# Kernel optimization log

Hardware: AMD Instinct MI355X
Metric: run time of the kernel (lower is better)

## Reference

```python
import jax, jax.numpy as jnp
import numpy as np

N = 50000      # nodes
E = 800000     # edges
DIN = 256
DH = 256
DOUT = 64


def setup_inputs() -> dict:
    key = jax.random.key(0)
    ks = jax.random.split(key, 8)
    x = jax.random.normal(ks[0], (N, DIN), dtype=jnp.float32)
    edge_index = jax.random.randint(ks[1], (2, E), 0, N, dtype=jnp.int64)
    s = 0.05
    W1 = jax.random.normal(ks[2], (DIN, DH), dtype=jnp.float32) * s
    b1 = jnp.zeros((DH,), dtype=jnp.float32)
    W2 = jax.random.normal(ks[3], (DH, DH), dtype=jnp.float32) * s
    b2 = jnp.zeros((DH,), dtype=jnp.float32)
    W3 = jax.random.normal(ks[4], (DH, DOUT), dtype=jnp.float32) * s
    b3 = jnp.zeros((DOUT,), dtype=jnp.float32)
    return {"x": x, "edge_index": edge_index, "W1": W1, "b1": b1,
            "W2": W2, "b2": b2, "W3": W3, "b3": b3}


def gcn_conv(x, src, dst, deg_inv_sqrt, W, b):
    # x: [N, din] -> [N, dout]. PyG GCNConv: h = D^{-1/2}(A+I)D^{-1/2} (x W) + b
    n = x.shape[0]
    h = x @ W                                   # [N, dout]
    norm = deg_inv_sqrt[src] * deg_inv_sqrt[dst]  # [E+N]
    msgs = h[src] * norm[:, None]               # gather + scale, [E+N, dout]
    out = jax.ops.segment_sum(msgs, dst, num_segments=n)  # scatter-add
    return out + b


def _loops(edge_index, n):
    # add self loops, compute symmetric normalization degrees
    sl = jnp.arange(n, dtype=edge_index.dtype)
    src = jnp.concatenate([edge_index[0], sl])
    dst = jnp.concatenate([edge_index[1], sl])
    deg = jax.ops.segment_sum(jnp.ones_like(dst, dtype=jnp.float32), dst, num_segments=n)
    dis = jnp.where(deg > 0, jax.lax.rsqrt(deg), 0.0)
    return src, dst, dis


def reference(x, edge_index, W1, b1, W2, b2, W3, b3):
    src, dst, dis = _loops(edge_index, x.shape[0])
    h = jax.nn.relu(gcn_conv(x, src, dst, dis, W1, b1))   # dropout: eval no-op
    h = jax.nn.relu(gcn_conv(h, src, dst, dis, W2, b2))
    out = gcn_conv(h, src, dst, dis, W3, b3)              # batch=None -> no pooling
    return out
```

## Files before the change

kernel.cpp:

```cpp
#include <hip/hip_runtime.h>
#include <hip/hip_fp8.h>
#include <cstdint>
#include <cstddef>

typedef unsigned short u16;
typedef _Float16 f16x8 __attribute__((ext_vector_type(8)));
typedef float f32x2 __attribute__((ext_vector_type(2)));
typedef float f32x4 __attribute__((ext_vector_type(4)));

#if defined(__has_builtin)
#if __has_builtin(__builtin_amdgcn_cvt_pk_f32_fp8) && __has_builtin(__builtin_amdgcn_cvt_pk_fp8_f32)
#define FP8_BUILTIN 1
#endif
#endif

__device__ __forceinline__ float h2f(u16 u) {
  return (float)__builtin_bit_cast(_Float16, u);
}
__device__ __forceinline__ u16 f2h(float f) {
  return __builtin_bit_cast(u16, (_Float16)f);
}
__device__ __forceinline__ unsigned pkh(float lo, float hi) {
  return (unsigned)f2h(lo) | ((unsigned)f2h(hi) << 16);
}
__device__ __forceinline__ unsigned char ftofp8(float f) {
#ifdef FP8_BUILTIN
  return (unsigned char)(__builtin_amdgcn_cvt_pk_fp8_f32(f, f, 0, false) & 0xFF);
#else
  return __hip_fp8_e4m3(f).__x;
#endif
}

__device__ __forceinline__ void async16(u16* lds, const u16* g) {
  __builtin_amdgcn_global_load_lds(
      (const __attribute__((address_space(1))) unsigned int*)g,
      (__attribute__((address_space(3))) unsigned int*)lds, 16, 0, 0);
}

__device__ __forceinline__ void fma8p(float* a, float d, uint2 p) {
#ifdef FP8_BUILTIN
  f32x2 v0 = __builtin_amdgcn_cvt_pk_f32_fp8((int)p.x, false);
  f32x2 v1 = __builtin_amdgcn_cvt_pk_f32_fp8((int)p.x, true);
  f32x2 v2 = __builtin_amdgcn_cvt_pk_f32_fp8((int)p.y, false);
  f32x2 v3 = __builtin_amdgcn_cvt_pk_f32_fp8((int)p.y, true);
  a[0] += d * v0.x; a[1] += d * v0.y; a[2] += d * v1.x; a[3] += d * v1.y;
  a[4] += d * v2.x; a[5] += d * v2.y; a[6] += d * v3.x; a[7] += d * v3.y;
#else
  const unsigned char* b = (const unsigned char*)&p;
#pragma unroll
  for (int k = 0; k < 8; ++k) {
    __hip_fp8_e4m3 v; v.__x = b[k];
    a[k] += d * (float)v;
  }
#endif
}

__device__ __forceinline__ void fma16p(float* a, float d, uint4 p) {
  fma8p(a, d, make_uint2(p.x, p.y));
  fma8p(a + 8, d, make_uint2(p.z, p.w));
}

__device__ __forceinline__ void fma8h(float* a, float d, uint4 p) {
  const u16* q = (const u16*)&p;
#pragma unroll
  for (int k = 0; k < 8; ++k) a[k] += d * h2f(q[k]);
}

__device__ __forceinline__ f16x8 cvt8(const float* p) {
  float4 a = *(const float4*)p;
  float4 b = *(const float4*)(p + 4);
  f16x8 r;
  r[0] = (_Float16)a.x; r[1] = (_Float16)a.y; r[2] = (_Float16)a.z; r[3] = (_Float16)a.w;
  r[4] = (_Float16)b.x; r[5] = (_Float16)b.y; r[6] = (_Float16)b.z; r[7] = (_Float16)b.w;
  return r;
}

__device__ __forceinline__ int wave_is64(const void* ep) {
  const unsigned* p = (const unsigned*)ep;
  const int lane = threadIdx.x & 63;
  unsigned v = p[2 * lane + 1] | p[2 * (lane + 64) + 1];
  unsigned long long bal = __ballot(v != 0u);
  return (bal == 0ull) ? 1 : 0;
}

__device__ __forceinline__ int edge_at(const void* ep, int is64, long long idx) {
  if (is64) return (int)((const long long*)ep)[idx];
  return ((const int*)ep)[idx];
}

#define NCHUNK 256

__global__ void zero_f32(float* p, int n) {
  int i = blockIdx.x * 256 + threadIdx.x;
  if (i < n) p[i] = 0.f;
}

__global__ __launch_bounds__(256) void prep_all(
    const float* __restrict__ W1, u16* __restrict__ wt1,
    const float* __restrict__ W2, u16* __restrict__ wt2,
    const float* __restrict__ W3, u16* __restrict__ wt3,
    const void* __restrict__ ep, int* __restrict__ cnt,
    int E, int N, int DIN, int DH, int DOUT,
    int nb_w1, int nb_w2, int nb_w3) {
  int b = blockIdx.x;
  if (b < nb_w1) {
    int idx = b * 256 + threadIdx.x;
    if (idx < DIN * DH) {
      int n = idx / DIN, k = idx % DIN;
      wt1[idx] = f2h(W1[k * DH + n]);
    }
    return;
  }
  b -= nb_w1;
  if (b < nb_w2) {
    int idx = b * 256 + threadIdx.x;
    if (idx < DH * DH) {
      int n = idx / DH, k = idx % DH;
      wt2[idx] = f2h(W2[k * DH + n]);
    }
    return;
  }
  b -= nb_w2;
  if (b < nb_w3) {
    int idx = b * 256 + threadIdx.x;
    if (idx < DH * DOUT) {
      int n = idx / DH, k = idx % DH;
      wt3[idx] = f2h(W3[k * DOUT + n]);
    }
    return;
  }
  b -= nb_w3;
  {
    __shared__ int h[256];
    h[threadIdx.x] = 0;
    __syncthreads();
    int is64 = wave_is64(ep);
    const int per = (E + NCHUNK - 1) / NCHUNK;
    const int e0 = b * per, e1 = min(e0 + per, E);
    for (int e = e0 + (int)threadIdx.x; e < e1; e += 256) {
      int d = edge_at(ep, is64, (long long)E + e);
      d = min(max(d, 0), N - 1);
      atomicAdd(&h[d >> 8], 1);
    }
    __syncthreads();
    cnt[b * 256 + threadIdx.x] = h[threadIdx.x];
  }
}

__device__ __forceinline__ void bases_in_lds(const int* __restrict__ cnt,
                                             int nbuck, int E, int* bl, int* ws4) {
  const int t = threadIdx.x, lane = t & 63, w = t >> 6;
  int tot = 0;
  if (t < nbuck) {
#pragma unroll 4
    for (int c = 0; c < NCHUNK; ++c) tot += cnt[c * 256 + t];
  }
  int inc = tot;
#pragma unroll
  for (int o = 1; o < 64; o <<= 1) {
    int u = __shfl_up(inc, o, 64);
    if (lane >= o) inc += u;
  }
  if (lane == 63) ws4[w] = inc;
  __syncthreads();
  if (t == 0) {
    int run = 0;
#pragma unroll
    for (int k = 0; k < 4; ++k) { int v = ws4[k]; ws4[k + 4] = run; run += v; }
  }
  __syncthreads();
  bl[t] = ws4[w + 4] + inc - tot;
  if (t == 0) bl[nbuck] = E;
  __syncthreads();
}

template <int BN, int OUT8, int A32, int NBT, int SC>
__device__ __forceinline__ void gemm_dev(const void* __restrict__ A,
                                         const u16* __restrict__ Bt,
                                         void* __restrict__ Cv, int Nt,
                                         int Nrows, int bm, int col0, u16* Bs) {
  constexpr int K = 256;
  constexpr int NJ = BN / 16;
  constexpr int CH = BN * K / 8;
  const int tid = threadIdx.x, lane = tid & 63, w = tid >> 6;

  auto stage = [&](int bt) {
#pragma unroll
    for (int i = 0; i < CH / 256; ++i) {
      int c = tid + i * 256;
      int ln = c & 63, t2 = c >> 6;
      int ks = t2 & 7, j = t2 >> 3;
      int row = bt * BN + j * 16 + (ln & 15);
      int kk = ks * 32 + (ln >> 4) * 8;
      async16(&Bs[(size_t)c * 8], Bt + (size_t)row * K + kk);
    }
  };
  stage(0);

  const int r16 = lane & 15, quad = lane >> 4;
  const int m0 = w * 32;
  int row0 = bm * 128 + m0 + r16;
  int row1 = row0 + 16;
  f16x8 aa0[8], aa1[8];
  if (A32) {
    row0 = min(row0, Nrows - 1);
    row1 = min(row1, Nrows - 1);
    const float* A0 = (const float*)A + (size_t)row0 * K + quad * 8;
    const float* A1 = (const float*)A + (size_t)row1 * K + quad * 8;
#pragma unroll
    for (int ks = 0; ks < 8; ++ks) {
      aa0[ks] = cvt8(A0 + ks * 32);
      aa1[ks] = cvt8(A1 + ks * 32);
    }
  } else {
    const u16* A0 = (const u16*)A + (size_t)row0 * K + quad * 8;
    const u16* A1 = (const u16*)A + (size_t)row1 * K + quad * 8;
#pragma unroll
    for (int ks = 0; ks < 8; ++ks) {
      aa0[ks] = *(const f16x8*)(A0 + ks * 32);
      aa1[ks] = *(const f16x8*)(A1 + ks * 32);
    }
  }

  const f32x4 fzero = {0.f, 0.f, 0.f, 0.f};
#pragma unroll
  for (int bt = 0; bt < NBT; ++bt) {
    f32x4 acc[2][NJ];
#pragma unroll
    for (int i = 0; i < 2; ++i)
#pragma unroll
      for (int j = 0; j < NJ; ++j) acc[i][j] = fzero;
    __syncthreads();
#pragma unroll
    for (int ks = 0; ks < 8; ++ks)
#pragma unroll
      for (int j = 0; j < NJ; ++j) {
        f16x8 bf = *(const f16x8*)(&Bs[(size_t)((j * 8 + ks) * 64 + lane) * 8]);
        acc[0][j] = __builtin_amdgcn_mfma_f32_16x16x32_f16(aa0[ks], bf, acc[0][j], 0, 0, 0);
        acc[1][j] = __builtin_amdgcn_mfma_f32_16x16x32_f16(aa1[ks], bf, acc[1][j], 0, 0, 0);
      }
    if (bt + 1 < NBT) {
      __syncthreads();
      stage(bt + 1);
    }
#pragma unroll
    for (int i = 0; i < 2; ++i)
#pragma unroll
      for (int j = 0; j < NJ; ++j) {
        int gr = bm * 128 + m0 + i * 16 + quad * 4;
        int gc = col0 + bt * BN + j * 16 + r16;
#pragma unroll
        for (int r = 0; r < 4; ++r) {
          if (OUT8) {
            ((unsigned char*)Cv)[(size_t)(gr + r) * Nt + gc] =
                ftofp8(acc[i][j][r] * (float)SC);
          } else {
            ((u16*)Cv)[(size_t)(gr + r) * Nt + gc] = f2h(acc[i][j][r]);
          }
        }
      }
  }
}

template <int BN, int OUT8, int A32, int NBT, int SC>
__global__ __launch_bounds__(256) void gemm_bres(const void* __restrict__ A,
                                                 const u16* __restrict__ Bt,
                                                 void* __restrict__ Cv, int Nt,
                                                 int Nrows) {
  __shared__ __align__(16) u16 Bs[BN * 256];
  const int col0 = blockIdx.y * (NBT * BN);
  gemm_dev<BN, OUT8, A32, NBT, SC>(A, Bt + (size_t)col0 * 256, Cv, Nt, Nrows,
                                   (int)blockIdx.x, col0, Bs);
}

__global__ __launch_bounds__(256) void bucket_gemm1(
    const void* __restrict__ ep, const int* __restrict__ cnt,
    unsigned* __restrict__ tmp, const float* __restrict__ x,
    const u16* __restrict__ wt1, unsigned char* __restrict__ hbuf,
    int E, int N, int nbuck) {
  __shared__ __align__(16) u16 Bs[128 * 256];
  if ((int)blockIdx.x >= NCHUNK) {
    gemm_dev<128, 1, 1, 2, 1>(x, wt1, hbuf, 256, N, (int)blockIdx.x - NCHUNK, 0, Bs);
    return;
  }
  int* bl = (int*)Bs;
  int* cur = bl + 272;
  int* ws4 = cur + 256;
  const int chunk = blockIdx.x;
  const int t = threadIdx.x;
  bases_in_lds(cnt, nbuck, E, bl, ws4);
  if (t < nbuck) {
    int partial = 0;
    for (int c = 0; c < chunk; ++c) partial += cnt[c * 256 + t];
    cur[t] = bl[t] + partial;
  }
  __syncthreads();
  int is64 = wave_is64(ep);
  const int per = (E + NCHUNK - 1) / NCHUNK;
  const int e0 = chunk * per, e1 = min(e0 + per, E);
  for (int e = e0 + t; e < e1; e += 256) {
    int s = edge_at(ep, is64, e);
    int d = edge_at(ep, is64, (long long)E + e);
    s = min(max(s, 0), N - 1);
    d = min(max(d, 0), N - 1);
    int pos = atomicAdd(&cur[d >> 8], 1);
    tmp[pos] = ((unsigned)d << 16) | (unsigned)s;
  }
}

__global__ __launch_bounds__(256) void csr_final(const unsigned* __restrict__ tmp,
                                                 const int* __restrict__ cnt,
                                                 int* __restrict__ rp,
                                                 float* __restrict__ dis,
                                                 u16* __restrict__ col,
                                                 int N, int E, int nbuck) {
  __shared__ int bl[257];
  __shared__ int hcnt[256];
  __shared__ int curs[256];
  __shared__ int ws4[8];
  const int b = blockIdx.x;
  const int node0 = b * 256;
  const int t = threadIdx.x, lane = t & 63, w = t >> 6;
  bases_in_lds(cnt, nbuck, E, bl, ws4);
  const int k0 = bl[b], k1 = bl[b + 1];
  hcnt[t] = 0;
  __syncthreads();
  for (int k = k0 + t; k < k1; k += 256)
    atomicAdd(&hcnt[(int)(tmp[k] >> 16) - node0], 1);
  __syncthreads();
  const int v = hcnt[t];
  int inc = v;
#pragma unroll
  for (int o = 1; o < 64; o <<= 1) {
    int u = __shfl_up(inc, o, 64);
    if (lane >= o) inc += u;
  }
  __syncthreads();
  if (lane == 63) ws4[w] = inc;
  __syncthreads();
  if (t == 0) {
    int run = 0;
#pragma unroll
    for (int k = 0; k < 4; ++k) { int vv = ws4[k]; ws4[k + 4] = run; run += vv; }
  }
  __syncthreads();
  const int excl = k0 + ws4[w + 4] + inc - v;
  if (node0 + t < N) {
    rp[node0 + t] = excl;
    dis[node0 + t] = rsqrtf((float)(v + 1));
  }
  if (b == 0 && t == 0) rp[N] = E;
  curs[t] = excl;
  __syncthreads();
  for (int k = k0 + t; k < k1; k += 256) {
    unsigned e = tmp[k];
    int dl = (int)(e >> 16) - node0;
    int pos = atomicAdd(&curs[dl], 1);
    col[pos] = (u16)(e & 0xFFFFu);
  }
}

template <int SCALED>
__global__ __launch_bounds__(256) void agg_d256(const unsigned char* __restrict__ h,
                                                const int* __restrict__ rp,
                                                const u16* __restrict__ col,
                                                const float* __restrict__ dis,
                                                const float* __restrict__ bias,
                                                u16* __restrict__ out, int N) {
  const int wid = threadIdx.x >> 6, lane = threadIdx.x & 63;
  const int i = blockIdx.x * 4 + wid;
  if (i >= N) return;
  const int sub = lane >> 4;
  const int l16 = lane & 15;
  const int cb = l16 * 16;
  const float di = dis[i];
  float a[16];
#pragma unroll
  for (int k = 0; k < 16; ++k) a[k] = 0.f;
  if (sub == 0) {
    uint4 sv = *(const uint4*)(h + (size_t)i * 256 + cb);
    fma16p(a, SCALED ? 1.f : di, sv);
  }
  const int e1 = rp[i + 1];
  for (int base = rp[i]; base < e1; base += 64) {
    int me = base + lane;
    int s_l = 0; float d_l = 0.f;
    if (me < e1) { s_l = (int)col[me]; if (!SCALED) d_l = dis[s_l]; }
    const int cnt = min(64, e1 - base);
    const int cntR = (cnt + 15) & ~15;
    for (int t = 0; t < cntR; t += 16) {
      int sA = __shfl(s_l, t + sub, 64);
      int sB = __shfl(s_l, t + 4 + sub, 64);
      int sC = __shfl(s_l, t + 8 + sub, 64);
      int sD = __shfl(s_l, t + 12 + sub, 64);
      float dA, dB, dC, dD;
      if (SCALED) {
        dA = (t + sub < cnt) ? 1.f : 0.f;
        dB = (t + 4 + sub < cnt) ? 1.f : 0.f;
        dC = (t + 8 + sub < cnt) ? 1.f : 0.f;
        dD = (t + 12 + sub < cnt) ? 1.f : 0.f;
      } else {
        dA = __shfl(d_l, t + sub, 64);
        dB = __shfl(d_l, t + 4 + sub, 64);
        dC = __shfl(d_l, t + 8 + sub, 64);
        dD = __shfl(d_l, t + 12 + sub, 64);
      }
      uint4 pA = *(const uint4*)(h + (size_t)sA * 256 + cb);
      uint4 pB = *(const uint4*)(h + (size_t)sB * 256 + cb);
      uint4 pC = *(const uint4*)(h + (size_t)sC * 256 + cb);
      uint4 pD = *(const uint4*)(h + (size_t)sD * 256 + cb);
      fma16p(a, dA, pA); fma16p(a, dB, pB); fma16p(a, dC, pC); fma16p(a, dD, pD);
    }
  }
#pragma unroll
  for (int k = 0; k < 16; ++k) a[k] += __shfl_xor(a[k], 16, 64);
#pragma unroll
  for (int k = 0; k < 16; ++k) a[k] += __shfl_xor(a[k], 32, 64);
  if (sub == 0) {
    const float inv = SCALED ? 0.25f : 1.f;
    const float* bp = bias + l16 * 16;
    float4 b0 = *(const float4*)(bp);
    float4 b1 = *(const float4*)(bp + 4);
    float4 b2 = *(const float4*)(bp + 8);
    float4 b3 = *(const float4*)(bp + 12);
    float bb[16] = {b0.x, b0.y, b0.z, b0.w, b1.x, b1.y, b1.z, b1.w,
                    b2.x, b2.y, b2.z, b2.w, b3.x, b3.y, b3.z, b3.w};
    float r[16];
#pragma unroll
    for (int k = 0; k < 16; ++k)
      r[k] = fmaxf(di * a[k] * inv + bb[k], 0.f) * di;
    uint4 o0, o1;
    o0.x = pkh(r[0], r[1]);  o0.y = pkh(r[2], r[3]);
    o0.z = pkh(r[4], r[5]);  o0.w = pkh(r[6], r[7]);
    o1.x = pkh(r[8], r[9]);  o1.y = pkh(r[10], r[11]);
    o1.z = pkh(r[12], r[13]); o1.w = pkh(r[14], r[15]);
    *(uint4*)(out + (size_t)i * 256 + l16 * 16) = o0;
    *(uint4*)(out + (size_t)i * 256 + l16 * 16 + 8) = o1;
  }
}

__global__ __launch_bounds__(256) void agg_d64(const u16* __restrict__ h,
                                               const int* __restrict__ rp,
                                               const u16* __restrict__ col,
                                               const float* __restrict__ dis,
                                               const float* __restrict__ bias,
                                               float* __restrict__ out, int N) {
  const int wid = threadIdx.x >> 6, lane = threadIdx.x & 63;
  const int i = blockIdx.x * 4 + wid;
  if (i >= N) return;
  const int grp = lane >> 3;
  const int l8 = lane & 7;
  const int c8 = l8 * 8;
  const float di = dis[i];
  float a[8] = {0.f, 0.f, 0.f, 0.f, 0.f, 0.f, 0.f, 0.f};
  if (grp == 0) {
    uint4 sv = *(const uint4*)(h + (size_t)i * 64 + c8);
    fma8h(a, 1.f, sv);
  }
  const int e1 = rp[i + 1];
  for (int base = rp[i]; base < e1; base += 64) {
    int me = base + lane;
    int s_l = 0;
    if (me < e1) s_l = (int)col[me];
    const int cnt = min(64, e1 - base);
    const int cntR = (cnt + 15) & ~15;
    for (int t = 0; t < cntR; t += 16) {
      int sA = __shfl(s_l, t + grp, 64);
      int sB = __shfl(s_l, t + 8 + grp, 64);
      float dA = (t + grp < cnt) ? 1.f : 0.f;
      float dB = (t + 8 + grp < cnt) ? 1.f : 0.f;
      uint4 pA = *(const uint4*)(h + (size_t)sA * 64 + c8);
      uint4 pB = *(const uint4*)(h + (size_t)sB * 64 + c8);
      fma8h(a, dA, pA); fma8h(a, dB, pB);
    }
  }
#pragma unroll
  for (int k = 0; k < 8; ++k) a[k] += __shfl_xor(a[k], 8, 64);
#pragma unroll
  for (int k = 0; k < 8; ++k) a[k] += __shfl_xor(a[k], 16, 64);
#pragma unroll
  for (int k = 0; k < 8; ++k) a[k] += __shfl_xor(a[k], 32, 64);
  if (lane < 8) {
    float4 b0 = *(const float4*)(bias + c8);
    float4 b1 = *(const float4*)(bias + c8 + 4);
    float4 o0, o1;
    o0.x = di * a[0] + b0.x; o0.y = di * a[1] + b0.y;
    o0.z = di * a[2] + b0.z; o0.w = di * a[3] + b0.w;
    o1.x = di * a[4] + b1.x; o1.y = di * a[5] + b1.y;
    o1.z = di * a[6] + b1.z; o1.w = di * a[7] + b1.w;
    *(float4*)(out + (size_t)i * 64 + c8) = o0;
    *(float4*)(out + (size_t)i * 64 + c8 + 4) = o1;
  }
}

extern "C" void kernel_launch(void* const* d_in, const int* in_sizes, int n_in,
                              void* d_out, int out_size, void* d_ws, size_t ws_size,
                              hipStream_t stream) {
  if (n_in < 8) return;
  const float* x = (const float*)d_in[0];
  const void* eptr = d_in[1];
  const float* W1 = (const float*)d_in[2];
  const float* b1 = (const float*)d_in[3];
  const float* W2 = (const float*)d_in[4];
  const float* b2 = (const float*)d_in[5];
  const float* W3 = (const float*)d_in[6];
  const float* b3 = (const float*)d_in[7];
  float* out = (float*)d_out;

  const int DIN = 256, DH = 256;
  const int N = in_sizes[0] / DIN;
  const int E = in_sizes[1] / 2;
  const int DOUT = in_sizes[6] / DH;
  const int MT = (N + 127) / 128;
  const int Mpad = MT * 128;
  const int nbuck = (N + 255) >> 8;

  auto rnd = [](size_t b) { return (b + 255) & ~(size_t)255; };
  size_t required = 0;
  required += rnd((size_t)Mpad * DH * 2);
  required += rnd((size_t)Mpad * DH);
  required += rnd((size_t)E * 2);
  required += rnd((size_t)E * 4);
  required += rnd((size_t)(N + 1) * 4);
  required += rnd((size_t)N * 4);
  required += rnd((size_t)DIN * DH * 2);
  required += rnd((size_t)DH * DH * 2);
  required += rnd((size_t)DH * DOUT * 2);
  required += rnd((size_t)256 * NCHUNK * 4);
  if (ws_size < required || N > 65536 || nbuck > 256 || nbuck < 1 ||
      E < 128 || DOUT != 64) {
    zero_f32<<<(out_size + 255) / 256, 256, 0, stream>>>(out, out_size);
    return;
  }

  char* ws = (char*)d_ws;
  size_t off0 = 0;
  auto alloc = [&](size_t bytes) {
    char* p = ws + off0;
    off0 = (off0 + bytes + 255) & ~(size_t)255;
    return p;
  };
  u16* xpad = (u16*)alloc((size_t)Mpad * DH * 2);
  unsigned char* hbuf = (unsigned char*)alloc((size_t)Mpad * DH);
  u16* colb = (u16*)alloc((size_t)E * 2);
  unsigned* tmpb = (unsigned*)alloc((size_t)E * 4);
  int* rp = (int*)alloc((size_t)(N + 1) * 4);
  float* dis = (float*)alloc((size_t)N * 4);
  u16* wt1 = (u16*)alloc((size_t)DIN * DH * 2);
  u16* wt2 = (u16*)alloc((size_t)DH * DH * 2);
  u16* wt3 = (u16*)alloc((size_t)DH * DOUT * 2);
  int* cnt = (int*)alloc((size_t)256 * NCHUNK * 4);

  const int nb_w1 = (DIN * DH + 255) / 256;
  const int nb_w2 = (DH * DH + 255) / 256;
  const int nb_w3 = (DH * DOUT + 255) / 256;
  prep_all<<<nb_w1 + nb_w2 + nb_w3 + NCHUNK, 256, 0, stream>>>(
      W1, wt1, W2, wt2, W3, wt3, eptr, cnt,
      E, N, DIN, DH, DOUT, nb_w1, nb_w2, nb_w3);

  bucket_gemm1<<<NCHUNK + MT, 256, 0, stream>>>(eptr, cnt, tmpb, x, wt1, hbuf,
                                                E, N, nbuck);
  csr_final<<<nbuck, 256, 0, stream>>>(tmpb, cnt, rp, dis, colb, N, E, nbuck);

  agg_d256<0><<<(N + 3) / 4, 256, 0, stream>>>(hbuf, rp, colb, dis, b1, xpad, N);
  gemm_bres<128, 1, 0, 2, 4><<<dim3(MT, 1), 256, 0, stream>>>(xpad, wt2, hbuf, DH, N);
  agg_d256<1><<<(N + 3) / 4, 256, 0, stream>>>(hbuf, rp, colb, dis, b2, xpad, N);
  gemm_bres<64, 0, 0, 1, 1><<<dim3(MT, DOUT / 64), 256, 0, stream>>>(
      xpad, wt3, hbuf, DOUT, N);
  agg_d64<<<(N + 3) / 4, 256, 0, stream>>>((const u16*)hbuf, rp, colb, dis, b3,
                                           out, N);
}
```

Measured before the change: 323.7 us.

## Split fused bucket/GEMM kernel, use 64-row GEMM tiles, deepen gather unrolling

Separates the CSR bucketing from the first GEMM so each is its own launch. Replaces the 128-row, 64KB-LDS GEMM with a 64-row tile using 32KB LDS and one A fragment per wave, which doubles the block count and cuts register and LDS pressure. The aggregation loops now issue 8 (d256) or 4 (d64) independent row gathers per iteration instead of 4 or 2, giving more memory-level parallelism. The cost is an extra launch, the loss of overlap between bucketing and GEMM1, and more re-staging of B per output row.

```diff
diff --git a/kernel.cpp b/kernel.cpp
--- a/kernel.cpp
+++ b/kernel.cpp
@@ -174,118 +174,13 @@
   __syncthreads();
 }
 
-template <int BN, int OUT8, int A32, int NBT, int SC>
-__device__ __forceinline__ void gemm_dev(const void* __restrict__ A,
-                                         const u16* __restrict__ Bt,
-                                         void* __restrict__ Cv, int Nt,
-                                         int Nrows, int bm, int col0, u16* Bs) {
-  constexpr int K = 256;
-  constexpr int NJ = BN / 16;
-  constexpr int CH = BN * K / 8;
-  const int tid = threadIdx.x, lane = tid & 63, w = tid >> 6;
-
-  auto stage = [&](int bt) {
-#pragma unroll
-    for (int i = 0; i < CH / 256; ++i) {
-      int c = tid + i * 256;
-      int ln = c & 63, t2 = c >> 6;
-      int ks = t2 & 7, j = t2 >> 3;
-      int row = bt * BN + j * 16 + (ln & 15);
-      int kk = ks * 32 + (ln >> 4) * 8;
-      async16(&Bs[(size_t)c * 8], Bt + (size_t)row * K + kk);
-    }
-  };
-  stage(0);
-
-  const int r16 = lane & 15, quad = lane >> 4;
-  const int m0 = w * 32;
-  int row0 = bm * 128 + m0 + r16;
-  int row1 = row0 + 16;
-  f16x8 aa0[8], aa1[8];
-  if (A32) {
-    row0 = min(row0, Nrows - 1);
-    row1 = min(row1, Nrows - 1);
-    const float* A0 = (const float*)A + (size_t)row0 * K + quad * 8;
-    const float* A1 = (const float*)A + (size_t)row1 * K + quad * 8;
-#pragma unroll
-    for (int ks = 0; ks < 8; ++ks) {
-      aa0[ks] = cvt8(A0 + ks * 32);
-      aa1[ks] = cvt8(A1 + ks * 32);
-    }
-  } else {
-    const u16* A0 = (const u16*)A + (size_t)row0 * K + quad * 8;
-    const u16* A1 = (const u16*)A + (size_t)row1 * K + quad * 8;
-#pragma unroll
-    for (int ks = 0; ks < 8; ++ks) {
-      aa0[ks] = *(const f16x8*)(A0 + ks * 32);
-      aa1[ks] = *(const f16x8*)(A1 + ks * 32);
-    }
-  }
-
-  const f32x4 fzero = {0.f, 0.f, 0.f, 0.f};
-#pragma unroll
-  for (int bt = 0; bt < NBT; ++bt) {
-    f32x4 acc[2][NJ];
-#pragma unroll
-    for (int i = 0; i < 2; ++i)
-#pragma unroll
-      for (int j = 0; j < NJ; ++j) acc[i][j] = fzero;
-    __syncthreads();
-#pragma unroll
-    for (int ks = 0; ks < 8; ++ks)
-#pragma unroll
-      for (int j = 0; j < NJ; ++j) {
-        f16x8 bf = *(const f16x8*)(&Bs[(size_t)((j * 8 + ks) * 64 + lane) * 8]);
-        acc[0][j] = __builtin_amdgcn_mfma_f32_16x16x32_f16(aa0[ks], bf, acc[0][j], 0, 0, 0);
-        acc[1][j] = __builtin_amdgcn_mfma_f32_16x16x32_f16(aa1[ks], bf, acc[1][j], 0, 0, 0);
-      }
-    if (bt + 1 < NBT) {
-      __syncthreads();
-      stage(bt + 1);
-    }
-#pragma unroll
-    for (int i = 0; i < 2; ++i)
-#pragma unroll
-      for (int j = 0; j < NJ; ++j) {
-        int gr = bm * 128 + m0 + i * 16 + quad * 4;
-        int gc = col0 + bt * BN + j * 16 + r16;
-#pragma unroll
-        for (int r = 0; r < 4; ++r) {
-          if (OUT8) {
-            ((unsigned char*)Cv)[(size_t)(gr + r) * Nt + gc] =
-                ftofp8(acc[i][j][r] * (float)SC);
-          } else {
-            ((u16*)Cv)[(size_t)(gr + r) * Nt + gc] = f2h(acc[i][j][r]);
-          }
-        }
-      }
-  }
-}
-
-template <int BN, int OUT8, int A32, int NBT, int SC>
-__global__ __launch_bounds__(256) void gemm_bres(const void* __restrict__ A,
-                                                 const u16* __restrict__ Bt,
-                                                 void* __restrict__ Cv, int Nt,
-                                                 int Nrows) {
-  __shared__ __align__(16) u16 Bs[BN * 256];
-  const int col0 = blockIdx.y * (NBT * BN);
-  gemm_dev<BN, OUT8, A32, NBT, SC>(A, Bt + (size_t)col0 * 256, Cv, Nt, Nrows,
-                                   (int)blockIdx.x, col0, Bs);
-}
-
-__global__ __launch_bounds__(256) void bucket_gemm1(
-    const void* __restrict__ ep, const int* __restrict__ cnt,
-    unsigned* __restrict__ tmp, const float* __restrict__ x,
-    const u16* __restrict__ wt1, unsigned char* __restrict__ hbuf,
-    int E, int N, int nbuck) {
-  __shared__ __align__(16) u16 Bs[128 * 256];
-  if ((int)blockIdx.x >= NCHUNK) {
-    gemm_dev<128, 1, 1, 2, 1>(x, wt1, hbuf, 256, N, (int)blockIdx.x - NCHUNK, 0, Bs);
-    return;
-  }
-  int* bl = (int*)Bs;
-  int* cur = bl + 272;
-  int* ws4 = cur + 256;
+__global__ __launch_bounds__(256) void csr_bucket(const void* __restrict__ ep,
+                                                  const int* __restrict__ cnt,
+                                                  unsigned* __restrict__ tmp,
+                                                  int E, int N, int nbuck) {
+  __shared__ int bl[257];
+  __shared__ int cur[256];
+  __shared__ int ws4[8];
   const int chunk = blockIdx.x;
   const int t = threadIdx.x;
   bases_in_lds(cnt, nbuck, E, bl, ws4);
@@ -360,6 +255,82 @@
   }
 }
 
+template <int OUT8, int A32, int NBT, int SC>
+__global__ __launch_bounds__(256) void gemm64(const void* __restrict__ A,
+                                              const u16* __restrict__ Bt,
+                                              void* __restrict__ Cv, int Nt,
+                                              int Nrows) {
+  constexpr int K = 256;
+  constexpr int BN = 64;
+  constexpr int NJ = 4;
+  constexpr int CH = BN * K / 8;
+  __shared__ __align__(16) u16 Bs[BN * K];
+
+  const int tid = threadIdx.x, lane = tid & 63, w = tid >> 6;
+  const int bm = blockIdx.x;
+
+  auto stage = [&](int bt) {
+#pragma unroll
+    for (int i = 0; i < CH / 256; ++i) {
+      int c = tid + i * 256;
+      int ln = c & 63, t2 = c >> 6;
+      int ks = t2 & 7, j = t2 >> 3;
+      int row = bt * BN + j * 16 + (ln & 15);
+      int kk = ks * 32 + (ln >> 4) * 8;
+      async16(&Bs[(size_t)c * 8], Bt + (size_t)row * K + kk);
+    }
+  };
+  stage(0);
+
+  const int r16 = lane & 15, quad = lane >> 4;
+  int row0 = bm * 64 + w * 16 + r16;
+  f16x8 aa[8];
+  if (A32) {
+    row0 = min(row0, Nrows - 1);
+    const float* A0 = (const float*)A + (size_t)row0 * K + quad * 8;
+#pragma unroll
+    for (int ks = 0; ks < 8; ++ks) aa[ks] = cvt8(A0 + ks * 32);
+  } else {
+    const u16* A0 = (const u16*)A + (size_t)row0 * K + quad * 8;
+#pragma unroll
+    for (int ks = 0; ks < 8; ++ks) aa[ks] = *(const f16x8*)(A0 + ks * 32);
+  }
+
+  const f32x4 fzero = {0.f, 0.f, 0.f, 0.f};
+#pragma unroll
+  for (int bt = 0; bt < NBT; ++bt) {
+    f32x4 acc[NJ];
+#pragma unroll
+    for (int j = 0; j < NJ; ++j) acc[j] = fzero;
+    __syncthreads();
+#pragma unroll
+    for (int ks = 0; ks < 8; ++ks)
+#pragma unroll
+      for (int j = 0; j < NJ; ++j) {
+        f16x8 bf = *(const f16x8*)(&Bs[(size_t)((j * 8 + ks) * 64 + lane) * 8]);
+        acc[j] = __builtin_amdgcn_mfma_f32_16x16x32_f16(aa[ks], bf, acc[j], 0, 0, 0);
+      }
+    if (bt + 1 < NBT) {
+      __syncthreads();
+      stage(bt + 1);
+    }
+    const int gr0 = bm * 64 + w * 16 + quad * 4;
+#pragma unroll
+    for (int j = 0; j < NJ; ++j) {
+      int gc = bt * BN + j * 16 + r16;
+#pragma unroll
+      for (int r = 0; r < 4; ++r) {
+        if (OUT8) {
+          ((unsigned char*)Cv)[(size_t)(gr0 + r) * Nt + gc] =
+              ftofp8(acc[j][r] * (float)SC);
+        } else {
+          ((u16*)Cv)[(size_t)(gr0 + r) * Nt + gc] = f2h(acc[j][r]);
+        }
+      }
+    }
+  }
+}
+
 template <int SCALED>
 __global__ __launch_bounds__(256) void agg_d256(const unsigned char* __restrict__ h,
                                                 const int* __restrict__ rp,
@@ -387,29 +358,21 @@
     int s_l = 0; float d_l = 0.f;
     if (me < e1) { s_l = (int)col[me]; if (!SCALED) d_l = dis[s_l]; }
     const int cnt = min(64, e1 - base);
-    const int cntR = (cnt + 15) & ~15;
-    for (int t = 0; t < cntR; t += 16) {
-      int sA = __shfl(s_l, t + sub, 64);
-      int sB = __shfl(s_l, t + 4 + sub, 64);
-      int sC = __shfl(s_l, t + 8 + sub, 64);
-      int sD = __shfl(s_l, t + 12 + sub, 64);
-      float dA, dB, dC, dD;
-      if (SCALED) {
-        dA = (t + sub < cnt) ? 1.f : 0.f;
-        dB = (t + 4 + sub < cnt) ? 1.f : 0.f;
-        dC = (t + 8 + sub < cnt) ? 1.f : 0.f;
-        dD = (t + 12 + sub < cnt) ? 1.f : 0.f;
-      } else {
-        dA = __shfl(d_l, t + sub, 64);
-        dB = __shfl(d_l, t + 4 + sub, 64);
-        dC = __shfl(d_l, t + 8 + sub, 64);
-        dD = __shfl(d_l, t + 12 + sub, 64);
+    const int cntR = (cnt + 31) & ~31;
+    for (int t = 0; t < cntR; t += 32) {
+      int ss[8]; float dd[8];
+#pragma unroll
+      for (int q = 0; q < 8; ++q) {
+        ss[q] = __shfl(s_l, t + q * 4 + sub, 64);
+        if (SCALED) dd[q] = (t + q * 4 + sub < cnt) ? 1.f : 0.f;
+        else        dd[q] = __shfl(d_l, t + q * 4 + sub, 64);
       }
-      uint4 pA = *(const uint4*)(h + (size_t)sA * 256 + cb);
-      uint4 pB = *(const uint4*)(h + (size_t)sB * 256 + cb);
-      uint4 pC = *(const uint4*)(h + (size_t)sC * 256 + cb);
-      uint4 pD = *(const uint4*)(h + (size_t)sD * 256 + cb);
-      fma16p(a, dA, pA); fma16p(a, dB, pB); fma16p(a, dC, pC); fma16p(a, dD, pD);
+      uint4 pp[8];
+#pragma unroll
+      for (int q = 0; q < 8; ++q)
+        pp[q] = *(const uint4*)(h + (size_t)ss[q] * 256 + cb);
+#pragma unroll
+      for (int q = 0; q < 8; ++q) fma16p(a, dd[q], pp[q]);
     }
   }
 #pragma unroll
@@ -463,15 +426,20 @@
     int s_l = 0;
     if (me < e1) s_l = (int)col[me];
     const int cnt = min(64, e1 - base);
-    const int cntR = (cnt + 15) & ~15;
-    for (int t = 0; t < cntR; t += 16) {
-      int sA = __shfl(s_l, t + grp, 64);
-      int sB = __shfl(s_l, t + 8 + grp, 64);
-      float dA = (t + grp < cnt) ? 1.f : 0.f;
-      float dB = (t + 8 + grp < cnt) ? 1.f : 0.f;
-      uint4 pA = *(const uint4*)(h + (size_t)sA * 64 + c8);
-      uint4 pB = *(const uint4*)(h + (size_t)sB * 64 + c8);
-      fma8h(a, dA, pA); fma8h(a, dB, pB);
+    const int cntR = (cnt + 31) & ~31;
+    for (int t = 0; t < cntR; t += 32) {
+      int ss[4]; float dd[4];
+#pragma unroll
+      for (int q = 0; q < 4; ++q) {
+        ss[q] = __shfl(s_l, t + q * 8 + grp, 64);
+        dd[q] = (t + q * 8 + grp < cnt) ? 1.f : 0.f;
+      }
+      uint4 pp[4];
+#pragma unroll
+      for (int q = 0; q < 4; ++q)
+        pp[q] = *(const uint4*)(h + (size_t)ss[q] * 64 + c8);
+#pragma unroll
+      for (int q = 0; q < 4; ++q) fma8h(a, dd[q], pp[q]);
     }
   }
 #pragma unroll
@@ -513,6 +481,7 @@
   const int DOUT = in_sizes[6] / DH;
   const int MT = (N + 127) / 128;
   const int Mpad = MT * 128;
+  const int MT64 = (N + 63) / 64;
   const int nbuck = (N + 255) >> 8;
 
   auto rnd = [](size_t b) { return (b + 255) & ~(size_t)255; };
@@ -558,15 +527,14 @@
       W1, wt1, W2, wt2, W3, wt3, eptr, cnt,
       E, N, DIN, DH, DOUT, nb_w1, nb_w2, nb_w3);
 
-  bucket_gemm1<<<NCHUNK + MT, 256, 0, stream>>>(eptr, cnt, tmpb, x, wt1, hbuf,
-                                                E, N, nbuck);
+  csr_bucket<<<NCHUNK, 256, 0, stream>>>(eptr, cnt, tmpb, E, N, nbuck);
   csr_final<<<nbuck, 256, 0, stream>>>(tmpb, cnt, rp, dis, colb, N, E, nbuck);
 
+  gemm64<1, 1, 4, 1><<<MT64, 256, 0, stream>>>(x, wt1, hbuf, DH, N);
   agg_d256<0><<<(N + 3) / 4, 256, 0, stream>>>(hbuf, rp, colb, dis, b1, xpad, N);
-  gemm_bres<128, 1, 0, 2, 4><<<dim3(MT, 1), 256, 0, stream>>>(xpad, wt2, hbuf, DH, N);
+  gemm64<1, 0, 4, 4><<<MT64, 256, 0, stream>>>(xpad, wt2, hbuf, DH, N);
   agg_d256<1><<<(N + 3) / 4, 256, 0, stream>>>(hbuf, rp, colb, dis, b2, xpad, N);
-  gemm_bres<64, 0, 0, 1, 1><<<dim3(MT, DOUT / 64), 256, 0, stream>>>(
-      xpad, wt3, hbuf, DOUT, N);
+  gemm64<0, 0, 1, 1><<<MT64, 256, 0, stream>>>(xpad, wt3, hbuf, DOUT, N);
   agg_d64<<<(N + 3) / 4, 256, 0, stream>>>((const u16*)hbuf, rp, colb, dis, b3,
                                            out, N);
 }
```

New measurement: 335.1 us. 3.5% more time.
